# Optimization experiments

Measured on AMD Instinct MI355X. Metric: run time of the kernel, lower is better.

The kernel has to match this reference:

```python
import jax, jax.numpy as jnp
import numpy as np

K = 3  # per_pix_kernel


def conv2d(x, w, b, pad):
    y = jax.lax.conv_general_dilated(
        x, w, window_strides=(1, 1), padding=[(pad, pad), (pad, pad)],
        dimension_numbers=('NCHW', 'OIHW', 'NCHW'))
    return y + b[None, :, None, None]


def per_pix_apply(x, kmap):
    # x: [B,C,H,W]; kmap: [B,K*K,H,W] (tanh-activated per-pixel kernels)
    # out[b,c,h,w] = sum_j patch_j(x)[b,c,h,w] * kmap[b,j,h,w]
    B, C, H, W = x.shape
    p = K // 2
    xp = jnp.pad(x, ((0, 0), (0, 0), (p, p), (p, p)))
    patches = jnp.stack(
        [xp[:, :, di:di + H, dj:dj + W] for di in range(K) for dj in range(K)],
        axis=1)  # [B, K*K, C, H, W]
    return jnp.einsum('bjchw,bjhw->bchw', patches, kmap)


def setup_inputs() -> dict:
    key = jax.random.key(0)
    ks = jax.random.split(key, 7)
    B, C, H, W = 4, 64, 256, 256
    kk = K * K  # 9
    s = 0.05
    return {
        'feature': jax.random.normal(ks[0], (B, C, H, W), jnp.float32),
        'w_sharp': jax.random.normal(ks[1], (kk, C, 5, 5), jnp.float32) * s,
        'b_sharp': jnp.zeros((kk,), jnp.float32),
        'w_r1': jax.random.normal(ks[2], (kk, C, 3, 3), jnp.float32) * s,
        'b_r1': jnp.zeros((kk,), jnp.float32),
        'w_r2': jax.random.normal(ks[3], (kk, kk, 3, 3), jnp.float32) * s,
        'b_r2': jnp.zeros((kk,), jnp.float32),
    }


def reference(feature, w_sharp, b_sharp, w_r1, b_r1, w_r2, b_r2):
    # sharp_attention = local_conv: 5x5 conv -> tanh -> per-pixel dynamic filter
    att_kernels = jnp.tanh(conv2d(feature, w_sharp, b_sharp, pad=2))  # [B,9,H,W]
    attention_feature = per_pix_apply(feature, att_kernels)           # [B,C,H,W]
    # reblur_filer (ratio == 1): conv3x3 -> conv3x3 -> tanh
    d = feature - attention_feature
    r = conv2d(d, w_r1, b_r1, pad=1)
    r = conv2d(r, w_r2, b_r2, pad=1)
    reblur_filter = jnp.tanh(r)  # [B,9,H,W]
    return reblur_filter, attention_feature
```

## Files before the change

### kernel.cpp

```cpp
#include <hip/hip_runtime.h>

#define B_ 4
#define C_ 64
#define H_ 256
#define W_ 256
#define KK 9

typedef __attribute__((ext_vector_type(8))) short short8;
typedef __attribute__((ext_vector_type(4))) float float4_;

static __device__ __forceinline__ unsigned short f2bf(float f) {
    unsigned int u = __builtin_bit_cast(unsigned int, f);
    unsigned int r = (u + 0x7fffu + ((u >> 16) & 1u)) >> 16;
    return (unsigned short)r;
}
static __device__ __forceinline__ float bf2f(short s) {
    return __builtin_bit_cast(float, (unsigned int)((unsigned short)s) << 16);
}
static __device__ __forceinline__ void gld16(const unsigned short* gp, unsigned short* lbase) {
    __builtin_amdgcn_global_load_lds(
        (const __attribute__((address_space(1))) unsigned int*)gp,
        (__attribute__((address_space(3))) unsigned int*)lbase, 16, 0, 0);
}
static __device__ __forceinline__ int att_idx(int pl, int j) {
    return (pl < 128) ? (pl * 9 + j) : (24320 + (pl - 128) * 9 + j);
}

__global__ __launch_bounds__(256) void nchw2nhwc(
    const float* __restrict__ x, unsigned short* __restrict__ xh)
{
    __shared__ unsigned short t[256 * 66];
    int row = blockIdx.x;
    int b = row >> 8;
    const float* src = x + ((size_t)b * 64) * 65536 + (size_t)(row & 255) * 256;
    int tid = threadIdx.x;

    #pragma unroll 8
    for (int c = 0; c < 64; c += 2) {
        unsigned int lo = f2bf(src[(size_t)c * 65536 + tid]);
        unsigned int hi = f2bf(src[(size_t)(c + 1) * 65536 + tid]);
        *(unsigned int*)(&t[tid * 66 + c]) = lo | (hi << 16);
    }
    __syncthreads();

    unsigned short* dst = xh + (size_t)row * 256 * 64;
    #pragma unroll
    for (int it = 0; it < 8; ++it) {
        int idx = it * 256 + tid;
        int pix = idx >> 3, g = idx & 7;
        short8 v = *(const short8*)(&t[pix * 66 + g * 8]);
        *(short8*)(dst + (size_t)pix * 64 + g * 8) = v;
    }
}

__global__ __launch_bounds__(256) void wprep_all(
    const float* __restrict__ w5, const float* __restrict__ w3,
    unsigned short* __restrict__ wb, unsigned short* __restrict__ wb3)
{
    int i = blockIdx.x * 256 + threadIdx.x;
    if (i < 25600) {
        int tap = i >> 10;
        int q = (i >> 7) & 7;
        int n = (i >> 3) & 15;
        int e = i & 7;
        int c = q * 8 + e;
        int di = tap / 5, dj = tap % 5;
        float v = (n < KK) ? w5[((n * C_ + c) * 5 + di) * 5 + dj] : 0.f;
        wb[i] = f2bf(v);
    } else if (i < 34816) {
        int k = i - 25600;
        int tap = k >> 10;
        int q = (k >> 7) & 7;
        int n = (k >> 3) & 15;
        int e = k & 7;
        int c = q * 8 + e;
        int di = tap / 3, dj = tap % 3;
        float v = (n < KK) ? w3[((n * C_ + c) * 3 + di) * 3 + dj] : 0.f;
        wb3[k] = f2bf(v);
    }
}

__global__ __launch_bounds__(512) void conv5_perpix(
    const unsigned short* __restrict__ xh,
    const unsigned short* __restrict__ wb,
    const float* __restrict__ bias,
    float* __restrict__ attf,
    unsigned short* __restrict__ dh)
{
    __shared__ __align__(16) unsigned short xs[20 * 20 * 64];

    int tid = threadIdx.x;
    int bx = blockIdx.x & 15;
    int by = (blockIdx.x >> 4) & 15;
    int b  = blockIdx.x >> 8;
    int h0 = by * 16, w0 = bx * 16;
    bool interior = (bx >= 1 && bx <= 14 && by >= 1 && by <= 14);

    int lane = tid & 63;
    int wid  = tid >> 6;

    if (interior) {
        int p = (lane & 7) ^ ((lane >> 3) & 7);
        for (int it = wid; it < 50; it += 8) {
            int pix = it * 8 + (lane >> 3);
            int py = pix / 20, px = pix % 20;
            int gy = h0 + py - 2, gx = w0 + px - 2;
            const unsigned short* g = xh + ((size_t)((b * 256 + gy) * 256 + gx) * 64 + p * 8);
            gld16(g, &xs[it * 512]);
        }
    } else {
        for (int q = tid; q < 400 * 8; q += 512) {
            int p = q & 7;
            int pix = q >> 3;
            int py = pix / 20, px = pix % 20;
            int gy = h0 + py - 2, gx = w0 + px - 2;
            short8 v = (short8)0;
            if (gy >= 0 && gy < H_ && gx >= 0 && gx < W_)
                v = *(const short8*)(xh + ((size_t)((b * 256 + gy) * 256 + gx) * 64 + p * 8));
            *(short8*)(&xs[(pix << 6) + ((p ^ (pix & 7)) << 3)]) = v;
        }
    }
    __syncthreads();

    int m16  = lane & 15;
    int lq   = lane >> 4;

    float4_ acc[2];
    float bj = (m16 < KK) ? bias[m16] : 0.f;
    #pragma unroll
    for (int r = 0; r < 2; ++r) acc[r] = (float4_){bj, bj, bj, bj};

    #pragma unroll
    for (int dj = 0; dj < 5; ++dj) {
        short8 bfr[5][2];
        #pragma unroll
        for (int di = 0; di < 5; ++di) {
            int tap = di * 5 + dj;
            bfr[di][0] = *(const short8*)(wb + (((tap * 8 + lq) * 16 + m16) * 8));
            bfr[di][1] = *(const short8*)(wb + (((tap * 8 + 4 + lq) * 16 + m16) * 8));
        }
        int px = m16 + dj;
        #pragma unroll
        for (int s = 0; s < 6; ++s) {
            int pix = (wid * 2 + s) * 20 + px;
            int c0 = lq ^ (pix & 7);
            short8 a0 = *(const short8*)(&xs[(pix << 6) + (c0 << 3)]);
            short8 a1 = *(const short8*)(&xs[(pix << 6) + ((c0 ^ 4) << 3)]);
            #pragma unroll
            for (int di = 0; di < 5; ++di) {
                int r = s - di;
                if (r < 0 || r > 1) continue;
                acc[r] = __builtin_amdgcn_mfma_f32_16x16x32_bf16(a0, bfr[di][0], acc[r], 0, 0, 0);
                acc[r] = __builtin_amdgcn_mfma_f32_16x16x32_bf16(a1, bfr[di][1], acc[r], 0, 0, 0);
            }
        }
    }
    __syncthreads();

    if (m16 < KK) {
        #pragma unroll
        for (int r = 0; r < 2; ++r) {
            #pragma unroll
            for (int reg = 0; reg < 4; ++reg) {
                int pl = (wid * 2 + r) * 16 + lq * 4 + reg;
                xs[att_idx(pl, m16)] = f2bf(tanhf(acc[r][reg]));
            }
        }
    }
    __syncthreads();

    #pragma unroll
    for (int it = 0; it < 4; ++it) {
        int idx = it * 512 + tid;
        int g = idx & 7;
        int pl = idx >> 3;
        int py = pl >> 4, px = pl & 15;
        int hw = ((h0 + py) << 8) | (w0 + px);

        float a[KK];
        #pragma unroll
        for (int j = 0; j < KK; ++j) a[j] = bf2f(xs[att_idx(pl, j)]);

        float s[8] = {0, 0, 0, 0, 0, 0, 0, 0};
        float xc[8] = {0, 0, 0, 0, 0, 0, 0, 0};
        #pragma unroll
        for (int di = 0; di < 3; ++di) {
            #pragma unroll
            for (int dj = 0; dj < 3; ++dj) {
                int tp = (py + 1 + di) * 20 + (px + 1 + dj);
                int c = g ^ (tp & 7);
                short8 v = *(const short8*)(&xs[(tp << 6) + (c << 3)]);
                float aj = a[di * 3 + dj];
                #pragma unroll
                for (int i = 0; i < 8; ++i) {
                    float xv = bf2f(v[i]);
                    s[i] += xv * aj;
                    if (di == 1 && dj == 1) xc[i] = xv;
                }
            }
        }

        #pragma unroll
        for (int i = 0; i < 8; ++i)
            attf[((b * C_ + g * 8 + i) << 16) | hw] = s[i];

        short8 dv;
        #pragma unroll
        for (int i = 0; i < 8; ++i) dv[i] = (short)f2bf(xc[i] - s[i]);
        *(short8*)(dh + ((size_t)((b << 16) | hw) * 64 + g * 8)) = dv;
    }
}

__global__ __launch_bounds__(512) void conv3_mfma(
    const unsigned short* __restrict__ dh,
    const unsigned short* __restrict__ wb3,
    const float* __restrict__ bias,
    unsigned short* __restrict__ r1h)
{
    __shared__ __align__(16) unsigned short xs[328 * 64];

    int tid = threadIdx.x;
    int bx = blockIdx.x & 15;
    int by = (blockIdx.x >> 4) & 15;
    int b  = blockIdx.x >> 8;
    int h0 = by * 16, w0 = bx * 16;
    bool interior = (bx >= 1 && bx <= 14 && by >= 1 && by <= 14);

    int lane = tid & 63;
    int wid  = tid >> 6;

    if (interior) {
        int p = (lane & 7) ^ ((lane >> 3) & 7);
        for (int it = wid; it < 41; it += 8) {
            int pix = it * 8 + (lane >> 3);
            int py = pix / 18, px = pix - py * 18;
            int gy = h0 + py - 1, gx = w0 + px - 1;
            const unsigned short* g = dh + ((size_t)((b * 256 + gy) * 256 + gx) * 64 + p * 8);
            gld16(g, &xs[it * 512]);
        }
    } else {
        for (int q = tid; q < 324 * 8; q += 512) {
            int p = q & 7;
            int pix = q >> 3;
            int py = pix / 18, px = pix - py * 18;
            int gy = h0 + py - 1, gx = w0 + px - 1;
            short8 v = (short8)0;
            if (gy >= 0 && gy < H_ && gx >= 0 && gx < W_)
                v = *(const short8*)(dh + ((size_t)((b * 256 + gy) * 256 + gx) * 64 + p * 8));
            *(short8*)(&xs[(pix << 6) + ((p ^ (pix & 7)) << 3)]) = v;
        }
    }
    __syncthreads();

    int m16  = lane & 15;
    int lq   = lane >> 4;

    float4_ acc[2];
    float bj = (m16 < KK) ? bias[m16] : 0.f;
    #pragma unroll
    for (int r = 0; r < 2; ++r) acc[r] = (float4_){bj, bj, bj, bj};

    #pragma unroll
    for (int dj = 0; dj < 3; ++dj) {
        short8 bfr[3][2];
        #pragma unroll
        for (int di = 0; di < 3; ++di) {
            int tap = di * 3 + dj;
            bfr[di][0] = *(const short8*)(wb3 + (((tap * 8 + lq) * 16 + m16) * 8));
            bfr[di][1] = *(const short8*)(wb3 + (((tap * 8 + 4 + lq) * 16 + m16) * 8));
        }
        int px = m16 + dj;
        #pragma unroll
        for (int s = 0; s < 4; ++s) {
            int pix = (wid * 2 + s) * 18 + px;
            int c0 = lq ^ (pix & 7);
            short8 a0 = *(const short8*)(&xs[(pix << 6) + (c0 << 3)]);
            short8 a1 = *(const short8*)(&xs[(pix << 6) + ((c0 ^ 4) << 3)]);
            #pragma unroll
            for (int di = 0; di < 3; ++di) {
                int r = s - di;
                if (r < 0 || r > 1) continue;
                acc[r] = __builtin_amdgcn_mfma_f32_16x16x32_bf16(a0, bfr[di][0], acc[r], 0, 0, 0);
                acc[r] = __builtin_amdgcn_mfma_f32_16x16x32_bf16(a1, bfr[di][1], acc[r], 0, 0, 0);
            }
        }
    }

    if (m16 < KK) {
        #pragma unroll
        for (int r = 0; r < 2; ++r) {
            int py = h0 + wid * 2 + r;
            #pragma unroll
            for (int reg = 0; reg < 4; ++reg) {
                int px = w0 + lq * 4 + reg;
                r1h[((b * KK + m16) << 16) | (py << 8) | px] = f2bf(acc[r][reg]);
            }
        }
    }
}

__global__ __launch_bounds__(256) void conv3_tanh9(
    const unsigned short* __restrict__ r1h, const float* __restrict__ w,
    const float* __restrict__ bias, float* __restrict__ out)
{
    const int TW = 32, TH = 8, PW = 34, PH = 10;
    __shared__ float lds[KK][PH][PW];

    int tid = threadIdx.x;
    int tx = tid & 31, ty = tid >> 5;
    int bw = blockIdx.x & 7;
    int bh = (blockIdx.x >> 3) & 31;
    int b  = blockIdx.x >> 8;
    int h0 = bh * TH, w0 = bw * TW;

    for (int idx = tid; idx < KK * PH * PW; idx += 256) {
        int px = idx % PW;
        int py = (idx / PW) % PH;
        int ch = idx / (PW * PH);
        int gy = h0 + py - 1, gx = w0 + px - 1;
        float v = 0.f;
        if (gy >= 0 && gy < H_ && gx >= 0 && gx < W_)
            v = bf2f(r1h[((b * KK + ch) << 16) | (gy << 8) | gx]);
        lds[ch][py][px] = v;
    }
    __syncthreads();

    float acc[KK];
    #pragma unroll
    for (int j = 0; j < KK; ++j) acc[j] = bias[j];

    for (int cin = 0; cin < KK; ++cin) {
        #pragma unroll
        for (int di = 0; di < 3; ++di) {
            #pragma unroll
            for (int dj = 0; dj < 3; ++dj) {
                float xv = lds[cin][ty + di][tx + dj];
                #pragma unroll
                for (int j = 0; j < KK; ++j)
                    acc[j] += xv * w[((j * KK + cin) * 3 + di) * 3 + dj];
            }
        }
    }

    int h = h0 + ty, wq = w0 + tx;
    #pragma unroll
    for (int j = 0; j < KK; ++j)
        out[((b * KK + j) << 16) | (h << 8) | wq] = tanhf(acc[j]);
}

extern "C" void kernel_launch(void* const* d_in, const int* in_sizes, int n_in,
                              void* d_out, int out_size, void* d_ws, size_t ws_size,
                              hipStream_t stream) {
    const float* feature = (const float*)d_in[0];
    const float* w_sharp = (const float*)d_in[1];
    const float* b_sharp = (const float*)d_in[2];
    const float* w_r1    = (const float*)d_in[3];
    const float* b_r1    = (const float*)d_in[4];
    const float* w_r2    = (const float*)d_in[5];
    const float* b_r2    = (const float*)d_in[6];

    float* out_reblur = (float*)d_out;
    float* out_attf   = out_reblur + (size_t)B_ * KK * H_ * W_;

    char* ws = (char*)d_ws;
    unsigned short* xh   = (unsigned short*)ws;
    unsigned short* dh   = (unsigned short*)(ws + 33554432);
    unsigned short* wb   = (unsigned short*)(ws + 67108864);
    unsigned short* wb3  = (unsigned short*)(ws + 67174400);
    unsigned short* r1h  = (unsigned short*)(ws + 67207168);

    nchw2nhwc<<<1024, 256, 0, stream>>>(feature, xh);
    wprep_all<<<136, 256, 0, stream>>>(w_sharp, w_r1, wb, wb3);
    conv5_perpix<<<1024, 512, 0, stream>>>(xh, wb, b_sharp, out_attf, dh);
    conv3_mfma<<<1024, 512, 0, stream>>>(dh, wb3, b_r1, r1h);
    conv3_tanh9<<<1024, 256, 0, stream>>>(r1h, w_r2, b_r2, out_reblur);
}
```

Before: 102.5 us.

## Fuse the two reblur 3x3 convs into one kernel with halo recompute

The first reblur conv (MFMA) and the second 9-channel conv plus tanh are merged into one kernel. Each block computes an 18x18 halo tile of the intermediate in LDS, zeroing out-of-image positions, then applies the second conv directly from LDS. This removes the r1h round trip through global memory and one launch, at the cost of extra halo MFMA work and a larger staging tile. Separately, the per-pixel apply now handles two adjacent pixels per thread, sharing the overlapping neighbour loads and writing float2 stores.

```diff
diff --git a/kernel.cpp b/kernel.cpp
--- a/kernel.cpp
+++ b/kernel.cpp
@@ -8,6 +8,7 @@
 
 typedef __attribute__((ext_vector_type(8))) short short8;
 typedef __attribute__((ext_vector_type(4))) float float4_;
+typedef __attribute__((ext_vector_type(2))) float float2_;
 
 static __device__ __forceinline__ unsigned short f2bf(float f) {
     unsigned int u = __builtin_bit_cast(unsigned int, f);
@@ -80,6 +81,34 @@
     }
 }
 
+static __device__ __forceinline__ void stage20(
+    const unsigned short* __restrict__ src, unsigned short* xs,
+    int b, int h0, int w0, bool interior, int tid)
+{
+    int lane = tid & 63, wid = tid >> 6;
+    if (interior) {
+        int p = (lane & 7) ^ ((lane >> 3) & 7);
+        for (int it = wid; it < 50; it += 8) {
+            int pix = it * 8 + (lane >> 3);
+            int py = pix / 20, px = pix % 20;
+            int gy = h0 + py - 2, gx = w0 + px - 2;
+            const unsigned short* g = src + ((size_t)((b * 256 + gy) * 256 + gx) * 64 + p * 8);
+            gld16(g, &xs[it * 512]);
+        }
+    } else {
+        for (int q = tid; q < 400 * 8; q += 512) {
+            int p = q & 7;
+            int pix = q >> 3;
+            int py = pix / 20, px = pix % 20;
+            int gy = h0 + py - 2, gx = w0 + px - 2;
+            short8 v = (short8)0;
+            if (gy >= 0 && gy < H_ && gx >= 0 && gx < W_)
+                v = *(const short8*)(src + ((size_t)((b * 256 + gy) * 256 + gx) * 64 + p * 8));
+            *(short8*)(&xs[(pix << 6) + ((p ^ (pix & 7)) << 3)]) = v;
+        }
+    }
+}
+
 __global__ __launch_bounds__(512) void conv5_perpix(
     const unsigned short* __restrict__ xh,
     const unsigned short* __restrict__ wb,
@@ -99,27 +128,7 @@
     int lane = tid & 63;
     int wid  = tid >> 6;
 
-    if (interior) {
-        int p = (lane & 7) ^ ((lane >> 3) & 7);
-        for (int it = wid; it < 50; it += 8) {
-            int pix = it * 8 + (lane >> 3);
-            int py = pix / 20, px = pix % 20;
-            int gy = h0 + py - 2, gx = w0 + px - 2;
-            const unsigned short* g = xh + ((size_t)((b * 256 + gy) * 256 + gx) * 64 + p * 8);
-            gld16(g, &xs[it * 512]);
-        }
-    } else {
-        for (int q = tid; q < 400 * 8; q += 512) {
-            int p = q & 7;
-            int pix = q >> 3;
-            int py = pix / 20, px = pix % 20;
-            int gy = h0 + py - 2, gx = w0 + px - 2;
-            short8 v = (short8)0;
-            if (gy >= 0 && gy < H_ && gx >= 0 && gx < W_)
-                v = *(const short8*)(xh + ((size_t)((b * 256 + gy) * 256 + gx) * 64 + p * 8));
-            *(short8*)(&xs[(pix << 6) + ((p ^ (pix & 7)) << 3)]) = v;
-        }
-    }
+    stage20(xh, xs, b, h0, w0, interior, tid);
     __syncthreads();
 
     int m16  = lane & 15;
@@ -170,54 +179,71 @@
     __syncthreads();
 
     #pragma unroll
-    for (int it = 0; it < 4; ++it) {
+    for (int it = 0; it < 2; ++it) {
         int idx = it * 512 + tid;
         int g = idx & 7;
-        int pl = idx >> 3;
-        int py = pl >> 4, px = pl & 15;
-        int hw = ((h0 + py) << 8) | (w0 + px);
-
-        float a[KK];
-        #pragma unroll
-        for (int j = 0; j < KK; ++j) a[j] = bf2f(xs[att_idx(pl, j)]);
-
-        float s[8] = {0, 0, 0, 0, 0, 0, 0, 0};
-        float xc[8] = {0, 0, 0, 0, 0, 0, 0, 0};
+        int grp = idx >> 3;
+        int py = grp >> 3;
+        int px0 = (grp & 7) * 2;
+        int pl0 = py * 16 + px0;
+
+        float a0[KK], a1[KK];
+        #pragma unroll
+        for (int j = 0; j < KK; ++j) {
+            a0[j] = bf2f(xs[att_idx(pl0, j)]);
+            a1[j] = bf2f(xs[att_idx(pl0 + 1, j)]);
+        }
+
+        float s0[8] = {0,0,0,0,0,0,0,0}, s1[8] = {0,0,0,0,0,0,0,0};
+        short8 cen0, cen1;
         #pragma unroll
         for (int di = 0; di < 3; ++di) {
+            short8 v[4];
+            #pragma unroll
+            for (int c = 0; c < 4; ++c) {
+                int tp = (py + 1 + di) * 20 + (px0 + 1 + c);
+                int cc = g ^ (tp & 7);
+                v[c] = *(const short8*)(&xs[(tp << 6) + (cc << 3)]);
+            }
+            if (di == 1) { cen0 = v[1]; cen1 = v[2]; }
             #pragma unroll
             for (int dj = 0; dj < 3; ++dj) {
-                int tp = (py + 1 + di) * 20 + (px + 1 + dj);
-                int c = g ^ (tp & 7);
-                short8 v = *(const short8*)(&xs[(tp << 6) + (c << 3)]);
-                float aj = a[di * 3 + dj];
+                float aj0 = a0[di * 3 + dj], aj1 = a1[di * 3 + dj];
                 #pragma unroll
                 for (int i = 0; i < 8; ++i) {
-                    float xv = bf2f(v[i]);
-                    s[i] += xv * aj;
-                    if (di == 1 && dj == 1) xc[i] = xv;
+                    s0[i] += bf2f(v[dj][i]) * aj0;
+                    s1[i] += bf2f(v[dj + 1][i]) * aj1;
                 }
             }
         }
 
-        #pragma unroll
-        for (int i = 0; i < 8; ++i)
-            attf[((b * C_ + g * 8 + i) << 16) | hw] = s[i];
-
-        short8 dv;
-        #pragma unroll
-        for (int i = 0; i < 8; ++i) dv[i] = (short)f2bf(xc[i] - s[i]);
-        *(short8*)(dh + ((size_t)((b << 16) | hw) * 64 + g * 8)) = dv;
-    }
-}
-
-__global__ __launch_bounds__(512) void conv3_mfma(
+        int hwb = ((h0 + py) << 8) | (w0 + px0);
+        #pragma unroll
+        for (int i = 0; i < 8; ++i) {
+            float2_ sv = {s0[i], s1[i]};
+            *(float2_*)(&attf[((b * C_ + g * 8 + i) << 16) | hwb]) = sv;
+        }
+        short8 dv0, dv1;
+        #pragma unroll
+        for (int i = 0; i < 8; ++i) {
+            dv0[i] = (short)f2bf(bf2f(cen0[i]) - s0[i]);
+            dv1[i] = (short)f2bf(bf2f(cen1[i]) - s1[i]);
+        }
+        unsigned short* dp = dh + ((size_t)((b << 16) | hwb) * 64 + g * 8);
+        *(short8*)dp = dv0;
+        *(short8*)(dp + 64) = dv1;
+    }
+}
+
+__global__ __launch_bounds__(512) void conv3_fused(
     const unsigned short* __restrict__ dh,
     const unsigned short* __restrict__ wb3,
-    const float* __restrict__ bias,
-    unsigned short* __restrict__ r1h)
+    const float* __restrict__ b1,
+    const float* __restrict__ w2,
+    const float* __restrict__ b2,
+    float* __restrict__ out)
 {
-    __shared__ __align__(16) unsigned short xs[328 * 64];
+    __shared__ __align__(16) unsigned short xs[20 * 20 * 64];
 
     int tid = threadIdx.x;
     int bx = blockIdx.x & 15;
@@ -229,36 +255,21 @@
     int lane = tid & 63;
     int wid  = tid >> 6;
 
-    if (interior) {
-        int p = (lane & 7) ^ ((lane >> 3) & 7);
-        for (int it = wid; it < 41; it += 8) {
-            int pix = it * 8 + (lane >> 3);
-            int py = pix / 18, px = pix - py * 18;
-            int gy = h0 + py - 1, gx = w0 + px - 1;
-            const unsigned short* g = dh + ((size_t)((b * 256 + gy) * 256 + gx) * 64 + p * 8);
-            gld16(g, &xs[it * 512]);
-        }
-    } else {
-        for (int q = tid; q < 324 * 8; q += 512) {
-            int p = q & 7;
-            int pix = q >> 3;
-            int py = pix / 18, px = pix - py * 18;
-            int gy = h0 + py - 1, gx = w0 + px - 1;
-            short8 v = (short8)0;
-            if (gy >= 0 && gy < H_ && gx >= 0 && gx < W_)
-                v = *(const short8*)(dh + ((size_t)((b * 256 + gy) * 256 + gx) * 64 + p * 8));
-            *(short8*)(&xs[(pix << 6) + ((p ^ (pix & 7)) << 3)]) = v;
-        }
-    }
+    stage20(dh, xs, b, h0, w0, interior, tid);
     __syncthreads();
 
     int m16  = lane & 15;
     int lq   = lane >> 4;
 
-    float4_ acc[2];
-    float bj = (m16 < KK) ? bias[m16] : 0.f;
-    #pragma unroll
-    for (int r = 0; r < 2; ++r) acc[r] = (float4_){bj, bj, bj, bj};
+    float4_ acc[2][2];
+    float4_ acc3[2];
+    float bj = (m16 < KK) ? b1[m16] : 0.f;
+    #pragma unroll
+    for (int st = 0; st < 2; ++st) {
+        acc3[st] = (float4_){bj, bj, bj, bj};
+        #pragma unroll
+        for (int r = 0; r < 2; ++r) acc[st][r] = (float4_){bj, bj, bj, bj};
+    }
 
     #pragma unroll
     for (int dj = 0; dj < 3; ++dj) {
@@ -269,83 +280,115 @@
             bfr[di][0] = *(const short8*)(wb3 + (((tap * 8 + lq) * 16 + m16) * 8));
             bfr[di][1] = *(const short8*)(wb3 + (((tap * 8 + 4 + lq) * 16 + m16) * 8));
         }
-        int px = m16 + dj;
-        #pragma unroll
-        for (int s = 0; s < 4; ++s) {
-            int pix = (wid * 2 + s) * 18 + px;
-            int c0 = lq ^ (pix & 7);
-            short8 a0 = *(const short8*)(&xs[(pix << 6) + (c0 << 3)]);
-            short8 a1 = *(const short8*)(&xs[(pix << 6) + ((c0 ^ 4) << 3)]);
+        int pxA = m16 + dj;
+        int pxB = m16 + dj + 2;
+        #pragma unroll
+        for (int sp = 0; sp < 4; ++sp) {
+            int row = wid * 2 + sp;
+            int pixA = row * 20 + pxA;
+            int cA = lq ^ (pixA & 7);
+            short8 aA0 = *(const short8*)(&xs[(pixA << 6) + (cA << 3)]);
+            short8 aA1 = *(const short8*)(&xs[(pixA << 6) + ((cA ^ 4) << 3)]);
+            int pixB = row * 20 + pxB;
+            int cB = lq ^ (pixB & 7);
+            short8 aB0 = *(const short8*)(&xs[(pixB << 6) + (cB << 3)]);
+            short8 aB1 = *(const short8*)(&xs[(pixB << 6) + ((cB ^ 4) << 3)]);
             #pragma unroll
             for (int di = 0; di < 3; ++di) {
-                int r = s - di;
+                int r = sp - di;
                 if (r < 0 || r > 1) continue;
-                acc[r] = __builtin_amdgcn_mfma_f32_16x16x32_bf16(a0, bfr[di][0], acc[r], 0, 0, 0);
-                acc[r] = __builtin_amdgcn_mfma_f32_16x16x32_bf16(a1, bfr[di][1], acc[r], 0, 0, 0);
-            }
-        }
-    }
+                acc[0][r] = __builtin_amdgcn_mfma_f32_16x16x32_bf16(aA0, bfr[di][0], acc[0][r], 0, 0, 0);
+                acc[0][r] = __builtin_amdgcn_mfma_f32_16x16x32_bf16(aA1, bfr[di][1], acc[0][r], 0, 0, 0);
+                acc[1][r] = __builtin_amdgcn_mfma_f32_16x16x32_bf16(aB0, bfr[di][0], acc[1][r], 0, 0, 0);
+                acc[1][r] = __builtin_amdgcn_mfma_f32_16x16x32_bf16(aB1, bfr[di][1], acc[1][r], 0, 0, 0);
+            }
+        }
+        if (wid < 2) {
+            #pragma unroll
+            for (int di = 0; di < 3; ++di) {
+                int row = 16 + wid + di;
+                int pixA = row * 20 + pxA;
+                int cA = lq ^ (pixA & 7);
+                short8 aA0 = *(const short8*)(&xs[(pixA << 6) + (cA << 3)]);
+                short8 aA1 = *(const short8*)(&xs[(pixA << 6) + ((cA ^ 4) << 3)]);
+                acc3[0] = __builtin_amdgcn_mfma_f32_16x16x32_bf16(aA0, bfr[di][0], acc3[0], 0, 0, 0);
+                acc3[0] = __builtin_amdgcn_mfma_f32_16x16x32_bf16(aA1, bfr[di][1], acc3[0], 0, 0, 0);
+                int pixB = row * 20 + pxB;
+                int cB = lq ^ (pixB & 7);
+                short8 aB0 = *(const short8*)(&xs[(pixB << 6) + (cB << 3)]);
+                short8 aB1 = *(const short8*)(&xs[(pixB << 6) + ((cB ^ 4) << 3)]);
+                acc3[1] = __builtin_amdgcn_mfma_f32_16x16x32_bf16(aB0, bfr[di][0], acc3[1], 0, 0, 0);
+                acc3[1] = __builtin_amdgcn_mfma_f32_16x16x32_bf16(aB1, bfr[di][1], acc3[1], 0, 0, 0);
+            }
+        }
+    }
+    __syncthreads();
 
     if (m16 < KK) {
         #pragma unroll
         for (int r = 0; r < 2; ++r) {
-            int py = h0 + wid * 2 + r;
+            int o = wid * 2 - 1 + r;
+            int gy = h0 + o;
             #pragma unroll
             for (int reg = 0; reg < 4; ++reg) {
-                int px = w0 + lq * 4 + reg;
-                r1h[((b * KK + m16) << 16) | (py << 8) | px] = f2bf(acc[r][reg]);
-            }
-        }
-    }
-}
-
-__global__ __launch_bounds__(256) void conv3_tanh9(
-    const unsigned short* __restrict__ r1h, const float* __restrict__ w,
-    const float* __restrict__ bias, float* __restrict__ out)
-{
-    const int TW = 32, TH = 8, PW = 34, PH = 10;
-    __shared__ float lds[KK][PH][PW];
-
-    int tid = threadIdx.x;
-    int tx = tid & 31, ty = tid >> 5;
-    int bw = blockIdx.x & 7;
-    int bh = (blockIdx.x >> 3) & 31;
-    int b  = blockIdx.x >> 8;
-    int h0 = bh * TH, w0 = bw * TW;
-
-    for (int idx = tid; idx < KK * PH * PW; idx += 256) {
-        int px = idx % PW;
-        int py = (idx / PW) % PH;
-        int ch = idx / (PW * PH);
-        int gy = h0 + py - 1, gx = w0 + px - 1;
-        float v = 0.f;
-        if (gy >= 0 && gy < H_ && gx >= 0 && gx < W_)
-            v = bf2f(r1h[((b * KK + ch) << 16) | (gy << 8) | gx]);
-        lds[ch][py][px] = v;
-    }
-    __syncthreads();
-
-    float acc[KK];
-    #pragma unroll
-    for (int j = 0; j < KK; ++j) acc[j] = bias[j];
-
-    for (int cin = 0; cin < KK; ++cin) {
+                int oc = lq * 4 + reg - 1;
+                int gx = w0 + oc;
+                float v = (gy >= 0 && gy < H_ && gx >= 0 && gx < W_) ? acc[0][r][reg] : 0.f;
+                xs[((o + 1) * 18 + (oc + 1)) * 24 + m16] = f2bf(v);
+            }
+            if (lq == 3) {
+                #pragma unroll
+                for (int reg = 2; reg < 4; ++reg) {
+                    int oc = 13 + reg;
+                    int gx = w0 + oc;
+                    float v = (gy >= 0 && gy < H_ && gx >= 0 && gx < W_) ? acc[1][r][reg] : 0.f;
+                    xs[((o + 1) * 18 + (oc + 1)) * 24 + m16] = f2bf(v);
+                }
+            }
+        }
+        if (wid < 2) {
+            int o = 15 + wid;
+            int gy = h0 + o;
+            #pragma unroll
+            for (int reg = 0; reg < 4; ++reg) {
+                int oc = lq * 4 + reg - 1;
+                int gx = w0 + oc;
+                float v = (gy >= 0 && gy < H_ && gx >= 0 && gx < W_) ? acc3[0][reg] : 0.f;
+                xs[((o + 1) * 18 + (oc + 1)) * 24 + m16] = f2bf(v);
+            }
+            if (lq == 3) {
+                #pragma unroll
+                for (int reg = 2; reg < 4; ++reg) {
+                    int oc = 13 + reg;
+                    int gx = w0 + oc;
+                    float v = (gy >= 0 && gy < H_ && gx >= 0 && gx < W_) ? acc3[1][reg] : 0.f;
+                    xs[((o + 1) * 18 + (oc + 1)) * 24 + m16] = f2bf(v);
+                }
+            }
+        }
+    }
+    __syncthreads();
+
+    for (int item = tid; item < 2304; item += 512) {
+        int cout = item >> 8;
+        int pl = item & 255;
+        int py = pl >> 4, px = pl & 15;
+        float acc2 = b2[cout];
         #pragma unroll
         for (int di = 0; di < 3; ++di) {
             #pragma unroll
             for (int dj = 0; dj < 3; ++dj) {
-                float xv = lds[cin][ty + di][tx + dj];
+                const unsigned short* rp = &xs[((py + di) * 18 + (px + dj)) * 24];
+                short8 rv = *(const short8*)rp;
+                float r8 = bf2f(rp[8]);
                 #pragma unroll
-                for (int j = 0; j < KK; ++j)
-                    acc[j] += xv * w[((j * KK + cin) * 3 + di) * 3 + dj];
-            }
-        }
-    }
-
-    int h = h0 + ty, wq = w0 + tx;
-    #pragma unroll
-    for (int j = 0; j < KK; ++j)
-        out[((b * KK + j) << 16) | (h << 8) | wq] = tanhf(acc[j]);
+                for (int cin = 0; cin < 8; ++cin)
+                    acc2 += bf2f(rv[cin]) * w2[((cout * KK + cin) * 3 + di) * 3 + dj];
+                acc2 += r8 * w2[((cout * KK + 8) * 3 + di) * 3 + dj];
+            }
+        }
+        out[((b * KK + cout) << 16) | ((h0 + py) << 8) | (w0 + px)] = tanhf(acc2);
+    }
 }
 
 extern "C" void kernel_launch(void* const* d_in, const int* in_sizes, int n_in,
@@ -367,11 +410,9 @@
     unsigned short* dh   = (unsigned short*)(ws + 33554432);
     unsigned short* wb   = (unsigned short*)(ws + 67108864);
     unsigned short* wb3  = (unsigned short*)(ws + 67174400);
-    unsigned short* r1h  = (unsigned short*)(ws + 67207168);
 
     nchw2nhwc<<<1024, 256, 0, stream>>>(feature, xh);
     wprep_all<<<136, 256, 0, stream>>>(w_sharp, w_r1, wb, wb3);
     conv5_perpix<<<1024, 512, 0, stream>>>(xh, wb, b_sharp, out_attf, dh);
-    conv3_mfma<<<1024, 512, 0, stream>>>(dh, wb3, b_r1, r1h);
-    conv3_tanh9<<<1024, 256, 0, stream>>>(r1h, w_r2, b_r2, out_reblur);
-}
+    conv3_fused<<<1024, 512, 0, stream>>>(dh, wb3, b_r1, w_r2, b_r2, out_reblur);
+}
```

After: 113.8 us. +11.0%, slower.
